# Performance work log

Measured on AMD Instinct MI355X. Metric: run time of the kernel, lower is better.

Reference implementation:

```python
import jax, jax.numpy as jnp
import numpy as np

N_QUBITS = 8
N_QLAYERS = 4
N_HEADS = 4
DIM = 2 ** N_QUBITS  # 256


def layer_norm(x, g, b, eps=1e-5):
    m = x.mean(-1, keepdims=True)
    v = ((x - m) ** 2).mean(-1, keepdims=True)
    return (x - m) / jnp.sqrt(v + eps) * g + b


def rx_mat(theta):
    # theta: scalar or [B]; returns [...,2,2] complex64
    h = theta * 0.5
    c = jnp.cos(h).astype(jnp.complex64)
    s = (jnp.sin(h) * (-1j)).astype(jnp.complex64)
    return jnp.stack([jnp.stack([c, s], -1), jnp.stack([s, c], -1)], -2)


def rz_mat(theta):
    h = (theta * 0.5).astype(jnp.complex64)
    e0 = jnp.exp(-1j * h)
    e1 = jnp.exp(1j * h)
    z = jnp.zeros_like(e0)
    return jnp.stack([jnp.stack([e0, z], -1), jnp.stack([z, e1], -1)], -2)


def apply_1q(state, U, wire, n):
    # state: [B, 2**n]; U: [2,2] (shared) or [B,2,2] (per-sample)
    B = state.shape[0]
    left = 2 ** wire
    right = 2 ** (n - 1 - wire)
    s = state.reshape(B, left, 2, right)
    if U.ndim == 2:
        s = jnp.einsum('jk,blkr->bljr', U, s)
    else:
        s = jnp.einsum('bjk,blkr->bljr', U, s)
    return s.reshape(B, 2 ** n)


def apply_cnot(state, ctrl, n):
    # CNOT with control=ctrl, target=ctrl+1 (adjacent wires)
    B = state.shape[0]
    left = 2 ** ctrl
    right = 2 ** (n - 2 - ctrl)
    s = state.reshape(B, left, 4, right)
    s = s[:, :, jnp.array([0, 1, 3, 2]), :]  # swap |10> and |11>
    return s.reshape(B, 2 ** n)


def quantum_expvals(angles, weights):
    # angles: [B, n_qubits] data-encoding angles; weights: [n_layers, 2, n_qubits]
    # Batched statevector sim of: RX(a_i)RZ(a_i) encoding, then per layer
    # RX(w[l,0,i]) RZ(w[l,1,i]) and a CNOT chain; returns <Z_i> per wire.
    n = N_QUBITS
    B = angles.shape[0]
    state = jnp.zeros((B, 2 ** n), jnp.complex64).at[:, 0].set(1.0)
    for i in range(n):
        state = apply_1q(state, rx_mat(angles[:, i]), i, n)
        state = apply_1q(state, rz_mat(angles[:, i]), i, n)
    for l in range(N_QLAYERS):
        for i in range(n):
            state = apply_1q(state, rx_mat(weights[l, 0, i]), i, n)
            state = apply_1q(state, rz_mat(weights[l, 1, i]), i, n)
        for i in range(n - 1):
            state = apply_cnot(state, i, n)
    probs = jnp.abs(state) ** 2  # [B, 2**n] float32
    zs = []
    for i in range(n):
        p = probs.reshape(B, 2 ** i, 2, 2 ** (n - 1 - i)).sum(axis=(1, 3))
        zs.append(p[:, 0] - p[:, 1])
    return jnp.stack(zs, -1)  # [B, n_qubits]


def mha(x, in_w, in_b, out_w, out_b):
    B, S, d = x.shape
    hd = d // N_HEADS
    qkv = x @ in_w.T + in_b  # [B,S,3d]
    q, k, v = jnp.split(qkv, 3, axis=-1)
    sp = lambda t: t.reshape(B, S, N_HEADS, hd).transpose(0, 2, 1, 3)
    q, k, v = sp(q), sp(k), sp(v)
    scores = jnp.einsum('bhqd,bhkd->bhqk', q, k) / np.sqrt(hd).astype(np.float32)
    attn = jax.nn.softmax(scores, axis=-1)
    o = jnp.einsum('bhqk,bhkd->bhqd', attn, v).transpose(0, 2, 1, 3).reshape(B, S, d)
    return o @ out_w.T + out_b


def _forward(x, attn_in_w, attn_in_b, attn_out_w, attn_out_b,
             ln1_g, ln1_b, ln2_g, ln2_b, ln3_g, ln3_b,
             qin_w, qin_b, qweights, qout_w, qout_b,
             ffn_w1, ffn_b1, ffn_w2, ffn_b2):
    attn_out = mha(x, attn_in_w, attn_in_b, attn_out_w, attn_out_b)
    x = layer_norm(x + attn_out, ln1_g, ln1_b)
    x_norm = layer_norm(x, ln3_g, ln3_b)
    B, S, d = x.shape
    flat = x_norm.reshape(B * S, d)
    angles = flat @ qin_w.T + qin_b  # [B*S, n_qubits]
    z = quantum_expvals(angles, qweights)
    q_out = (z @ qout_w.T + qout_b).reshape(B, S, d)
    x = x + q_out
    h = jax.nn.gelu(x @ ffn_w1.T + ffn_b1, approximate=False)  # torch GELU exact
    ffn_out = h @ ffn_w2.T + ffn_b2  # dropout is identity in eval
    return layer_norm(x + ffn_out, ln2_g, ln2_b)


def setup_inputs() -> dict:
    key = jax.random.key(0)
    ks = jax.random.split(key, 10)
    B, S, d, nq, nl = 32, 512, 512, N_QUBITS, N_QLAYERS
    rn = lambda k, sh, sc=0.02: jax.random.normal(k, sh, jnp.float32) * sc
    return {
        'x': jax.random.normal(ks[0], (B, S, d), jnp.float32),
        'attn_in_w': rn(ks[1], (3 * d, d)),
        'attn_in_b': jnp.zeros((3 * d,), jnp.float32),
        'attn_out_w': rn(ks[2], (d, d)),
        'attn_out_b': jnp.zeros((d,), jnp.float32),
        'ln1_g': jnp.ones((d,), jnp.float32), 'ln1_b': jnp.zeros((d,), jnp.float32),
        'ln2_g': jnp.ones((d,), jnp.float32), 'ln2_b': jnp.zeros((d,), jnp.float32),
        'ln3_g': jnp.ones((d,), jnp.float32), 'ln3_b': jnp.zeros((d,), jnp.float32),
        'qin_w': rn(ks[3], (nq, d), 0.05),
        'qin_b': jnp.zeros((nq,), jnp.float32),
        'qweights': jax.random.uniform(ks[4], (nl, 2, nq), jnp.float32, 0.0, 2.0 * np.pi),
        'qout_w': rn(ks[5], (d, nq), 0.1),
        'qout_b': jnp.zeros((d,), jnp.float32),
        'ffn_w1': rn(ks[6], (4 * d, d)),
        'ffn_b1': jnp.zeros((4 * d,), jnp.float32),
        'ffn_w2': rn(ks[7], (d, 4 * d)),
        'ffn_b2': jnp.zeros((d,), jnp.float32),
    }


def reference(x, attn_in_w, attn_in_b, attn_out_w, attn_out_b,
              ln1_g, ln1_b, ln2_g, ln2_b, ln3_g, ln3_b,
              qin_w, qin_b, qweights, qout_w, qout_b,
              ffn_w1, ffn_b1, ffn_w2, ffn_b2):
    return _forward(x, attn_in_w, attn_in_b, attn_out_w, attn_out_b,
                    ln1_g, ln1_b, ln2_g, ln2_b, ln3_g, ln3_b,
                    qin_w, qin_b, qweights, qout_w, qout_b,
                    ffn_w1, ffn_b1, ffn_w2, ffn_b2)
```

## Files before the change

### kernel.cpp

```cpp
#include <hip/hip_runtime.h>
#include <math.h>


typedef __bf16 bf16;
typedef bf16 bf16x8 __attribute__((ext_vector_type(8)));
typedef bf16 bf16x4 __attribute__((ext_vector_type(4)));
typedef float f32x4 __attribute__((ext_vector_type(4)));

__device__ __forceinline__ void gld16(const void* g, void* l) {
  __builtin_amdgcn_global_load_lds(
      (__attribute__((address_space(1))) void*)(void*)g,
      (__attribute__((address_space(3))) void*)l, 16, 0, 0);
}

__device__ __forceinline__ float waveAllSum(float v) {
#pragma unroll
  for (int m = 1; m < 64; m <<= 1) v += __shfl_xor(v, m, 64);
  return v;
}

__global__ __launch_bounds__(256) void cvt_all(
    const float* __restrict__ x, const float* __restrict__ w1,
    const float* __restrict__ w2, const float* __restrict__ w3,
    const float* __restrict__ w4, bf16* __restrict__ xb,
    bf16* __restrict__ b1, bf16* __restrict__ b2, bf16* __restrict__ b3,
    bf16* __restrict__ b4) {
  int i = blockIdx.x * 256 + threadIdx.x;
  const float* src;
  bf16* dst;
  int off;
  if (i < 2097152) {
    src = x; dst = xb; off = i;
  } else if (i < 2097152 + 196608) {
    src = w1; dst = b1; off = i - 2097152;
  } else if (i < 2097152 + 196608 + 65536) {
    src = w2; dst = b2; off = i - (2097152 + 196608);
  } else if (i < 2097152 + 196608 + 65536 + 262144) {
    src = w3; dst = b3; off = i - (2097152 + 196608 + 65536);
  } else {
    src = w4; dst = b4; off = i - (2097152 + 196608 + 65536 + 262144);
  }
  float4 v = ((const float4*)src)[off];
  bf16x4 o = {(bf16)v.x, (bf16)v.y, (bf16)v.z, (bf16)v.w};
  ((bf16x4*)dst)[off] = o;
}

__global__ void make_gates(const float* __restrict__ qw,
                           float* __restrict__ gates) {
  int t = threadIdx.x;
  if (t >= 32) return;
  int l = t >> 3, i = t & 7;
  float ax = qw[l * 16 + i] * 0.5f;
  float az = qw[l * 16 + 8 + i] * 0.5f;
  float cx, sx, cz, sz;
  sincosf(ax, &sx, &cx);
  sincosf(az, &sz, &cz);
  float* g = gates + t * 8;
  g[0] = cz * cx;   g[1] = -sz * cx;
  g[2] = -sz * sx;  g[3] = -cz * sx;
  g[4] = sz * sx;   g[5] = -cz * sx;
  g[6] = cz * cx;   g[7] = sz * cx;
}

__global__ __launch_bounds__(256) void make_W(const float* __restrict__ gates,
                                              bf16* __restrict__ Wp) {
  int tid = threadIdx.x, lane = tid & 63;
  int k = blockIdx.x * 4 + (tid >> 6);

  float sr[4], si[4];
#pragma unroll
  for (int l = 0; l < 4; ++l) {
    sr[l] = (lane * 4 + l == k) ? 1.0f : 0.0f;
    si[l] = 0.0f;
  }

  auto gate = [&](int p, float u00r, float u00i, float u01r, float u01i,
                  float u10r, float u10i, float u11r, float u11i) {
    if (p >= 2) {
      int m = 1 << (p - 2);
      int b = (lane >> (p - 2)) & 1;
      float csr = b ? u11r : u00r;
      float csi = b ? u11i : u00i;
      float cor = b ? u10r : u01r;
      float coi = b ? u10i : u01i;
#pragma unroll
      for (int l = 0; l < 4; ++l) {
        float pr = __shfl_xor(sr[l], m, 64);
        float pi = __shfl_xor(si[l], m, 64);
        float nr = fmaf(csr, sr[l],
                        fmaf(-csi, si[l], fmaf(cor, pr, -coi * pi)));
        float ni = fmaf(csr, si[l],
                        fmaf(csi, sr[l], fmaf(cor, pi, coi * pr)));
        sr[l] = nr;
        si[l] = ni;
      }
    } else {
      float nr[4], ni[4];
#pragma unroll
      for (int l = 0; l < 4; ++l) {
        int b = (l >> p) & 1;
        int pl = l ^ (1 << p);
        float csr = b ? u11r : u00r;
        float csi = b ? u11i : u00i;
        float cor = b ? u10r : u01r;
        float coi = b ? u10i : u01i;
        nr[l] = fmaf(csr, sr[l],
                     fmaf(-csi, si[l], fmaf(cor, sr[pl], -coi * si[pl])));
        ni[l] = fmaf(csr, si[l],
                     fmaf(csi, sr[l], fmaf(cor, si[pl], coi * sr[pl])));
      }
#pragma unroll
      for (int l = 0; l < 4; ++l) {
        sr[l] = nr[l];
        si[l] = ni[l];
      }
    }
  };
  auto docnot = [&](int i) {
    int pc = 7 - i, pt = 6 - i;
    if (pt >= 2) {
      int ctrl = (lane >> (pc - 2)) & 1;
      int m = 1 << (pt - 2);
#pragma unroll
      for (int l = 0; l < 4; ++l) {
        float pr = __shfl_xor(sr[l], m, 64);
        float pi = __shfl_xor(si[l], m, 64);
        if (ctrl) {
          sr[l] = pr;
          si[l] = pi;
        }
      }
    } else if (pt == 1) {
      if (lane & 1) {
        float t;
        t = sr[0]; sr[0] = sr[2]; sr[2] = t;
        t = si[0]; si[0] = si[2]; si[2] = t;
        t = sr[1]; sr[1] = sr[3]; sr[3] = t;
        t = si[1]; si[1] = si[3]; si[3] = t;
      }
    } else {
      float t;
      t = sr[2]; sr[2] = sr[3]; sr[3] = t;
      t = si[2]; si[2] = si[3]; si[3] = t;
    }
  };

  for (int l = 0; l < 4; ++l) {
    for (int i = 0; i < 8; ++i) {
      const float* g = gates + (l * 8 + i) * 8;
      gate(7 - i, g[0], g[1], g[2], g[3], g[4], g[5], g[6], g[7]);
    }
    for (int i = 0; i < 7; ++i) docnot(i);
  }

#pragma unroll
  for (int l = 0; l < 4; ++l) {
    int j = lane * 4 + l;
    Wp[j * 512 + k] = (bf16)sr[l];
    Wp[j * 512 + 256 + k] = (bf16)(-si[l]);
    Wp[(j + 256) * 512 + k] = (bf16)si[l];
    Wp[(j + 256) * 512 + 256 + k] = (bf16)sr[l];
  }
}

__global__ __launch_bounds__(256) void make_Q(const float* __restrict__ qout_w,
                                              bf16* __restrict__ Q) {
  int t = blockIdx.x * 256 + threadIdx.x;
  int col = t >> 8, k = t & 255;
  float s = 0.f;
#pragma unroll
  for (int w = 0; w < 8; ++w) {
    float sg = ((k >> (7 - w)) & 1) ? -1.0f : 1.0f;
    s = fmaf(qout_w[col * 8 + w], sg, s);
  }
  Q[col * 256 + k] = (bf16)s;
}

__global__ __launch_bounds__(256) void gemm_mfma(
    const bf16* __restrict__ A, const bf16* __restrict__ W,
    const float* __restrict__ bias, const float* __restrict__ Xadd,
    float* __restrict__ Cf, bf16* __restrict__ Cb, bf16* __restrict__ qk,
    bf16* __restrict__ vT, int M, int N, int K, int mode) {
  __shared__ __align__(16) bf16 As[128 * 64];
  __shared__ __align__(16) bf16 Bs[128 * 64];
  int tid = threadIdx.x;
  int lane = tid & 63, w = tid >> 6;
  int wr = w >> 1, wc = w & 1;
  int quad = lane >> 4, lc = lane & 15;
  long m0 = (long)blockIdx.x * 128;
  long n0 = (long)blockIdx.y * 128;
  f32x4 acc[4][4] = {};

  int sl0 = w * 256 + lane;

  for (int k0 = 0; k0 < K; k0 += 64) {
    __syncthreads();
#pragma unroll
    for (int c = 0; c < 4; ++c) {
      int slot = sl0 + c * 64;
      int row = slot >> 3, g = slot & 7;
      int sc = (g ^ (row & 7)) << 3;
      gld16(A + (m0 + row) * (long)K + k0 + sc, &As[slot << 3]);
      gld16(W + (n0 + row) * (long)K + k0 + sc, &Bs[slot << 3]);
    }
    __syncthreads();
#pragma unroll
    for (int t = 0; t < 2; ++t) {
      bf16x8 af[4], bfr[4];
      int pg = ((t * 4 + quad) ^ (lc & 7)) << 3;
#pragma unroll
      for (int i = 0; i < 4; ++i) {
        af[i] = *(const bf16x8*)&As[(wr * 64 + i * 16 + lc) * 64 + pg];
        bfr[i] = *(const bf16x8*)&Bs[(wc * 64 + i * 16 + lc) * 64 + pg];
      }
#pragma unroll
      for (int i = 0; i < 4; ++i)
#pragma unroll
        for (int j = 0; j < 4; ++j)
          acc[i][j] = __builtin_amdgcn_mfma_f32_16x16x32_bf16(
              af[i], bfr[j], acc[i][j], 0, 0, 0);
    }
  }

#pragma unroll
  for (int i = 0; i < 4; ++i) {
    long grow0 = m0 + wr * 64 + i * 16 + quad * 4;
#pragma unroll
    for (int j = 0; j < 4; ++j) {
      long col = n0 + wc * 64 + j * 16 + lc;
      float bv = (mode == 3) ? 0.f : bias[col];
      float v[4];
#pragma unroll
      for (int r = 0; r < 4; ++r) v[r] = acc[i][j][r] + bv;
      if (mode == 0) {
#pragma unroll
        for (int r = 0; r < 4; ++r) Cf[(grow0 + r) * N + col] = v[r];
      } else if (mode == 1) {
#pragma unroll
        for (int r = 0; r < 4; ++r) {
          float g = 0.5f * v[r] * (1.0f + erff(v[r] * 0.70710678118654752f));
          Cb[(grow0 + r) * N + col] = (bf16)g;
        }
      } else if (mode == 3) {
#pragma unroll
        for (int r = 0; r < 4; ++r) Cb[(grow0 + r) * N + col] = (bf16)v[r];
      } else if (mode == 4) {
#pragma unroll
        for (int r = 0; r < 4; ++r) {
          float val = v[r] + Xadd[(grow0 + r) * N + col];
          Cf[(grow0 + r) * N + col] = val;
          Cb[(grow0 + r) * N + col] = (bf16)val;
        }
      } else {
        if (col < 1024) {
#pragma unroll
          for (int r = 0; r < 4; ++r) qk[(grow0 + r) * 1024 + col] = (bf16)v[r];
        } else {
          int hh = (int)((col - 1024) >> 7);
          int dd = (int)((col - 1024) & 127);
          long bidx = grow0 >> 9;
          int s0 = (int)(grow0 & 511);
          bf16x4 pk = {(bf16)v[0], (bf16)v[1], (bf16)v[2], (bf16)v[3]};
          *(bf16x4*)&vT[(((bidx << 2) + hh) * 128 + dd) * 512 + s0] = pk;
        }
      }
    }
  }
}

__global__ __launch_bounds__(256) void attn_mfma(const bf16* __restrict__ qk,
                                                 const bf16* __restrict__ vT,
                                                 bf16* __restrict__ o) {
  __shared__ __align__(16) bf16 Ks[64 * 128];
  __shared__ __align__(16) bf16 Vt[128 * 64];
  __shared__ __align__(16) bf16 Ps[4][64 * 16];
  int tid = threadIdx.x, lane = tid & 63, w = tid >> 6;
  int quad = lane >> 4, lc = lane & 15;
  int bh = blockIdx.x, b = bh >> 2, h = bh & 3;
  int q0 = blockIdx.y * 64 + w * 16;
  const float scale = 0.08838834764831845f;

  bf16x8 qf[4];
  {
    const bf16* qp =
        qk + ((long)(b * 512 + q0 + lc)) * 1024 + h * 128 + quad * 8;
#pragma unroll
    for (int ks = 0; ks < 4; ++ks) qf[ks] = *(const bf16x8*)(qp + ks * 32);
  }
  f32x4 oacc[8] = {};
  float lrun[4] = {0.f, 0.f, 0.f, 0.f};

  const bf16* kbase = qk + (long)b * 512 * 1024 + 512 + h * 128;
  const bf16* vbase = vT + (long)bh * 128 * 512;
  int sl0 = w * 256 + lane;

  for (int kt = 0; kt < 512; kt += 64) {
    __syncthreads();
#pragma unroll
    for (int c = 0; c < 4; ++c) {
      int slot = sl0 + c * 64;
      {
        int row = slot >> 4, g = slot & 15;
        gld16(kbase + (long)(kt + row) * 1024 + ((g ^ (row & 15)) << 3),
              &Ks[slot << 3]);
      }
      {
        int row = slot >> 3, g = slot & 7;
        gld16(vbase + (long)row * 512 + kt + ((g ^ (row & 7)) << 3),
              &Vt[slot << 3]);
      }
    }
    __syncthreads();

    float p[4][4];
#pragma unroll
    for (int c = 0; c < 4; ++c) {
      f32x4 a = {};
#pragma unroll
      for (int ks = 0; ks < 4; ++ks) {
        bf16x8 kf = *(const bf16x8*)&Ks[(c * 16 + lc) * 128 +
                                        (((ks * 4 + quad) ^ lc) << 3)];
        a = __builtin_amdgcn_mfma_f32_16x16x32_bf16(qf[ks], kf, a, 0, 0, 0);
      }
#pragma unroll
      for (int r = 0; r < 4; ++r) p[c][r] = a[r] * scale;
    }

#pragma unroll
    for (int r = 0; r < 4; ++r) {
      float rs = 0.f;
#pragma unroll
      for (int c = 0; c < 4; ++c) {
        float e = expf(p[c][r]);
        p[c][r] = e;
        rs += e;
      }
#pragma unroll
      for (int m = 1; m < 16; m <<= 1) rs += __shfl_xor(rs, m, 64);
      lrun[r] += rs;
    }

#pragma unroll
    for (int c = 0; c < 4; ++c) {
      bf16x4 pk = {(bf16)p[c][0], (bf16)p[c][1], (bf16)p[c][2], (bf16)p[c][3]};
      *(bf16x4*)&Ps[w][(c * 16 + lc) * 16 + ((quad ^ (lc & 3)) << 2)] = pk;
    }
    bf16x8 pf[2];
#pragma unroll
    for (int kc = 0; kc < 2; ++kc) {
      bf16x8 t;
#pragma unroll
      for (int jj = 0; jj < 8; ++jj) {
        int row = kc * 32 + quad * 8 + jj;
        t[jj] = Ps[w][row * 16 + (((lc >> 2) ^ (row & 3)) << 2) + (lc & 3)];
      }
      pf[kc] = t;
    }
#pragma unroll
    for (int n = 0; n < 8; ++n)
#pragma unroll
      for (int kc = 0; kc < 2; ++kc) {
        bf16x8 vf = *(const bf16x8*)&Vt[(n * 16 + lc) * 64 +
                                        (((kc * 4 + quad) ^ (lc & 7)) << 3)];
        oacc[n] =
            __builtin_amdgcn_mfma_f32_16x16x32_bf16(pf[kc], vf, oacc[n], 0, 0, 0);
      }
  }

  float linv[4];
#pragma unroll
  for (int r = 0; r < 4; ++r) linv[r] = 1.0f / lrun[r];
  bf16* op = o + ((long)(b * 512 + q0 + quad * 4)) * 512 + h * 128 + lc;
#pragma unroll
  for (int n = 0; n < 8; ++n)
#pragma unroll
    for (int r = 0; r < 4; ++r)
      op[(long)r * 512 + n * 16] = (bf16)(oacc[n][r] * linv[r]);
}

__global__ __launch_bounds__(256) void add_ln_kernel(
    const float* __restrict__ a, const float* __restrict__ b,
    const float* __restrict__ g, const float* __restrict__ be,
    float* __restrict__ out) {
  long row = (blockIdx.x * 256 + threadIdx.x) >> 6;
  int lane = threadIdx.x & 63;
  const float* ar = a + row * 512;
  const float* br = b + row * 512;
  float v[8];
  float s = 0.f;
#pragma unroll
  for (int j = 0; j < 8; ++j) {
    int c = lane + 64 * j;
    v[j] = ar[c] + br[c];
    s += v[j];
  }
  s = waveAllSum(s);
  float mean = s * (1.0f / 512.0f);
  float var = 0.f;
#pragma unroll
  for (int j = 0; j < 8; ++j) {
    float d = v[j] - mean;
    var = fmaf(d, d, var);
  }
  var = waveAllSum(var);
  float rstd = rsqrtf(var * (1.0f / 512.0f) + 1e-5f);
  float* orow = out + row * 512;
#pragma unroll
  for (int j = 0; j < 8; ++j) {
    int c = lane + 64 * j;
    orow[c] = (v[j] - mean) * rstd * g[c] + be[c];
  }
}

__global__ __launch_bounds__(256) void quantum_pre(
    const float* __restrict__ x, const float* __restrict__ attnp,
    const float* __restrict__ g1, const float* __restrict__ b1,
    const float* __restrict__ g3, const float* __restrict__ b3,
    const float* __restrict__ qin_w, const float* __restrict__ qin_b,
    float* __restrict__ x1out, bf16* __restrict__ psi) {
  long row = (blockIdx.x * 256 + threadIdx.x) >> 6;
  int lane = threadIdx.x & 63;
  const float* xr = x + row * 512;
  const float* ar = attnp + row * 512;

  float x1v[8];
  {
    float s = 0.f;
#pragma unroll
    for (int j = 0; j < 8; ++j) {
      int c = lane + 64 * j;
      x1v[j] = xr[c] + ar[c];
      s += x1v[j];
    }
    s = waveAllSum(s);
    float mean = s * (1.0f / 512.0f);
    float var = 0.f;
#pragma unroll
    for (int j = 0; j < 8; ++j) {
      float d = x1v[j] - mean;
      var = fmaf(d, d, var);
    }
    var = waveAllSum(var);
    float rstd = rsqrtf(var * (1.0f / 512.0f) + 1e-5f);
#pragma unroll
    for (int j = 0; j < 8; ++j) {
      int c = lane + 64 * j;
      x1v[j] = (x1v[j] - mean) * rstd * g1[c] + b1[c];
    }
  }
  float* x1row = x1out + row * 512;
#pragma unroll
  for (int j = 0; j < 8; ++j) x1row[lane + 64 * j] = x1v[j];

  float xn[8];
  {
    float s = 0.f;
#pragma unroll
    for (int j = 0; j < 8; ++j) s += x1v[j];
    s = waveAllSum(s);
    float mean = s * (1.0f / 512.0f);
    float var = 0.f;
#pragma unroll
    for (int j = 0; j < 8; ++j) {
      float d = x1v[j] - mean;
      var = fmaf(d, d, var);
    }
    var = waveAllSum(var);
    float rstd = rsqrtf(var * (1.0f / 512.0f) + 1e-5f);
#pragma unroll
    for (int j = 0; j < 8; ++j) {
      int c = lane + 64 * j;
      xn[j] = (x1v[j] - mean) * rstd * g3[c] + b3[c];
    }
  }

  float ang[8];
#pragma unroll
  for (int w = 0; w < 8; ++w) {
    float p = 0.f;
#pragma unroll
    for (int j = 0; j < 8; ++j)
      p = fmaf(xn[j], qin_w[w * 512 + lane + 64 * j], p);
    p = waveAllSum(p);
    ang[w] = p + qin_b[w];
  }

  float v0r[8], v0i[8], v1r[8];
#pragma unroll
  for (int i = 0; i < 8; ++i) {
    float h = ang[i] * 0.5f;
    float c, s;
    sincosf(h, &s, &c);
    v0r[i] = c * c;
    v0i[i] = -c * s;
    v1r[i] = s * s;
  }

  float Pr, Pi;
  {
    int bit0 = (lane >> 5) & 1;
    Pr = bit0 ? v1r[0] : v0r[0];
    Pi = v0i[0];
#pragma unroll
    for (int i = 1; i < 6; ++i) {
      int bit = (lane >> (5 - i)) & 1;
      float br = bit ? v1r[i] : v0r[i];
      float bi = v0i[i];
      float nr = Pr * br - Pi * bi;
      float ni = Pr * bi + Pi * br;
      Pr = nr;
      Pi = ni;
    }
  }

  bf16 rebuf[4], imbuf[4];
#pragma unroll
  for (int l = 0; l < 4; ++l) {
    int b6 = (l >> 1) & 1, b7 = l & 1;
    float br = b6 ? v1r[6] : v0r[6], bi = v0i[6];
    float tr = Pr * br - Pi * bi;
    float ti = Pr * bi + Pi * br;
    float cr = b7 ? v1r[7] : v0r[7], ci = v0i[7];
    float fr = tr * cr - ti * ci;
    float fi = tr * ci + ti * cr;
    rebuf[l] = (bf16)fr;
    imbuf[l] = (bf16)fi;
  }
  bf16* prow = psi + row * 512;
  *(bf16x4*)&prow[lane * 4] = *(bf16x4*)rebuf;
  *(bf16x4*)&prow[256 + lane * 4] = *(bf16x4*)imbuf;
}

__global__ __launch_bounds__(256) void prob_kernel(const bf16* __restrict__ phi,
                                                   bf16* __restrict__ prob) {
  int t4 = blockIdx.x * 256 + threadIdx.x;
  int token = t4 >> 6;
  int k4 = (t4 & 63) * 4;
  const bf16* pr = phi + (long)token * 512;
  bf16x4 re = *(const bf16x4*)&pr[k4];
  bf16x4 im = *(const bf16x4*)&pr[256 + k4];
  bf16 ob[4];
#pragma unroll
  for (int l = 0; l < 4; ++l) {
    float r = (float)re[l], i = (float)im[l];
    ob[l] = (bf16)(r * r + i * i);
  }
  *(bf16x4*)&prob[(long)token * 256 + k4] = *(bf16x4*)ob;
}

extern "C" void kernel_launch(void* const* d_in, const int* in_sizes, int n_in,
                              void* d_out, int out_size, void* d_ws,
                              size_t ws_size, hipStream_t stream) {
  const float* x = (const float*)d_in[0];
  const float* attn_in_w = (const float*)d_in[1];
  const float* attn_in_b = (const float*)d_in[2];
  const float* attn_out_w = (const float*)d_in[3];
  const float* attn_out_b = (const float*)d_in[4];
  const float* ln1_g = (const float*)d_in[5];
  const float* ln1_b = (const float*)d_in[6];
  const float* ln2_g = (const float*)d_in[7];
  const float* ln2_b = (const float*)d_in[8];
  const float* ln3_g = (const float*)d_in[9];
  const float* ln3_b = (const float*)d_in[10];
  const float* qin_w = (const float*)d_in[11];
  const float* qin_b = (const float*)d_in[12];
  const float* qweights = (const float*)d_in[13];
  const float* qout_w = (const float*)d_in[14];
  const float* qout_b = (const float*)d_in[15];
  const float* ffn_w1 = (const float*)d_in[16];
  const float* ffn_b1 = (const float*)d_in[17];
  const float* ffn_w2 = (const float*)d_in[18];
  const float* ffn_b2 = (const float*)d_in[19];

  char* wsB = (char*)d_ws;
  bf16* qkb = (bf16*)(wsB);
  bf16* vtb = (bf16*)(wsB + (32L << 20));
  bf16* ob = (bf16*)(wsB + (48L << 20));
  bf16* hb = (bf16*)(wsB);
  float* slot1 = (float*)(wsB + (64L << 20));
  bf16* phi = (bf16*)(wsB + (64L << 20));
  bf16* probb = (bf16*)(wsB + (80L << 20));
  float* f2out = (float*)(wsB + (64L << 20));
  float* x1 = (float*)(wsB + (96L << 20));
  float* x2 = (float*)(wsB + (128L << 20));
  bf16* x2b = (bf16*)(wsB + (160L << 20));
  bf16* xb = (bf16*)(wsB + (176L << 20));
  bf16* psi = (bf16*)(wsB + (176L << 20));
  bf16* w_in = (bf16*)(wsB + (192L << 20));
  bf16* w_out = (bf16*)(wsB + (194L << 20));
  bf16* w_f1 = (bf16*)(wsB + (195L << 20));
  bf16* w_f2 = (bf16*)(wsB + (197L << 20));
  float* gates = (float*)(wsB + (199L << 20));
  bf16* Wp = (bf16*)(wsB + (200L << 20));
  bf16* Qm = (bf16*)(wsB + (201L << 20));

  const int M = 16384;
  float* outp = (float*)d_out;

  cvt_all<<<11264, 256, 0, stream>>>(x, attn_in_w, attn_out_w, ffn_w1, ffn_w2,
                                     xb, w_in, w_out, w_f1, w_f2);
  make_gates<<<1, 64, 0, stream>>>(qweights, gates);
  make_W<<<64, 256, 0, stream>>>(gates, Wp);
  make_Q<<<512, 256, 0, stream>>>(qout_w, Qm);

  gemm_mfma<<<dim3(M / 128, 12), 256, 0, stream>>>(
      xb, w_in, attn_in_b, nullptr, nullptr, nullptr, qkb, vtb, M, 1536, 512,
      2);
  attn_mfma<<<dim3(128, 8), 256, 0, stream>>>(qkb, vtb, ob);
  gemm_mfma<<<dim3(M / 128, 4), 256, 0, stream>>>(
      ob, w_out, attn_out_b, nullptr, slot1, nullptr, nullptr, nullptr, M, 512,
      512, 0);
  quantum_pre<<<dim3(M / 4), 256, 0, stream>>>(x, slot1, ln1_g, ln1_b, ln3_g,
                                               ln3_b, qin_w, qin_b, x1, psi);
  gemm_mfma<<<dim3(M / 128, 4), 256, 0, stream>>>(
      psi, Wp, nullptr, nullptr, nullptr, phi, nullptr, nullptr, M, 512, 512,
      3);
  prob_kernel<<<4096, 256, 0, stream>>>(phi, probb);
  gemm_mfma<<<dim3(M / 128, 4), 256, 0, stream>>>(
      probb, Qm, qout_b, x1, x2, x2b, nullptr, nullptr, M, 512, 256, 4);
  gemm_mfma<<<dim3(M / 128, 16), 256, 0, stream>>>(
      x2b, w_f1, ffn_b1, nullptr, nullptr, hb, nullptr, nullptr, M, 2048, 512,
      1);
  gemm_mfma<<<dim3(M / 128, 4), 256, 0, stream>>>(
      hb, w_f2, ffn_b2, nullptr, f2out, nullptr, nullptr, nullptr, M, 512,
      2048, 0);
  add_ln_kernel<<<dim3(M / 4), 256, 0, stream>>>(x2, f2out, ln2_g, ln2_b,
                                                 outp);
}
```

Before: 463.6 us.

## Store intermediates in bf16, fuse prob into GEMM, merge gate setup, fast GELU

All fp32 intermediates (attention projection, x1, x2, FFN output) become bf16, roughly halving their global memory traffic. The prob kernel is folded into the psi×W GEMM epilogue by interleaving real and imaginary rows and summing squares with a lane shuffle. make_gates is merged into make_W, and erf GELU is replaced by a tanh-style approximation using __expf, with softmax also switched to __expf. The cost is lower precision in the residual path and an approximate GELU, which may push results past the tolerance.

Measured after the change: 428.4 us. 1.08x faster.

```diff
diff --git a/kernel.cpp b/kernel.cpp
--- a/kernel.cpp
+++ b/kernel.cpp
@@ -17,6 +17,11 @@
 #pragma unroll
   for (int m = 1; m < 64; m <<= 1) v += __shfl_xor(v, m, 64);
   return v;
+}
+
+__device__ __forceinline__ float fast_gelu(float v) {
+  float u = 0.79788456080286536f * v * (1.0f + 0.044715f * v * v);
+  return v / (1.0f + __expf(-2.0f * u));
 }
 
 __global__ __launch_bounds__(256) void cvt_all(
@@ -45,26 +50,24 @@
   ((bf16x4*)dst)[off] = o;
 }
 
-__global__ void make_gates(const float* __restrict__ qw,
-                           float* __restrict__ gates) {
-  int t = threadIdx.x;
-  if (t >= 32) return;
-  int l = t >> 3, i = t & 7;
-  float ax = qw[l * 16 + i] * 0.5f;
-  float az = qw[l * 16 + 8 + i] * 0.5f;
-  float cx, sx, cz, sz;
-  sincosf(ax, &sx, &cx);
-  sincosf(az, &sz, &cz);
-  float* g = gates + t * 8;
-  g[0] = cz * cx;   g[1] = -sz * cx;
-  g[2] = -sz * sx;  g[3] = -cz * sx;
-  g[4] = sz * sx;   g[5] = -cz * sx;
-  g[6] = cz * cx;   g[7] = sz * cx;
-}
-
-__global__ __launch_bounds__(256) void make_W(const float* __restrict__ gates,
+__global__ __launch_bounds__(256) void make_W(const float* __restrict__ qw,
                                               bf16* __restrict__ Wp) {
+  __shared__ float gates[32 * 8];
   int tid = threadIdx.x, lane = tid & 63;
+  if (tid < 32) {
+    int l = tid >> 3, i = tid & 7;
+    float ax = qw[l * 16 + i] * 0.5f;
+    float az = qw[l * 16 + 8 + i] * 0.5f;
+    float cx, sx, cz, sz;
+    sincosf(ax, &sx, &cx);
+    sincosf(az, &sz, &cz);
+    float* g = gates + tid * 8;
+    g[0] = cz * cx;   g[1] = -sz * cx;
+    g[2] = -sz * sx;  g[3] = -cz * sx;
+    g[4] = sz * sx;   g[5] = -cz * sx;
+    g[6] = cz * cx;   g[7] = sz * cx;
+  }
+  __syncthreads();
   int k = blockIdx.x * 4 + (tid >> 6);
 
   float sr[4], si[4];
@@ -156,10 +159,10 @@
 #pragma unroll
   for (int l = 0; l < 4; ++l) {
     int j = lane * 4 + l;
-    Wp[j * 512 + k] = (bf16)sr[l];
-    Wp[j * 512 + 256 + k] = (bf16)(-si[l]);
-    Wp[(j + 256) * 512 + k] = (bf16)si[l];
-    Wp[(j + 256) * 512 + 256 + k] = (bf16)sr[l];
+    Wp[(2 * j) * 512 + k] = (bf16)sr[l];
+    Wp[(2 * j) * 512 + 256 + k] = (bf16)(-si[l]);
+    Wp[(2 * j + 1) * 512 + k] = (bf16)si[l];
+    Wp[(2 * j + 1) * 512 + 256 + k] = (bf16)sr[l];
   }
 }
 
@@ -178,9 +181,9 @@
 
 __global__ __launch_bounds__(256) void gemm_mfma(
     const bf16* __restrict__ A, const bf16* __restrict__ W,
-    const float* __restrict__ bias, const float* __restrict__ Xadd,
-    float* __restrict__ Cf, bf16* __restrict__ Cb, bf16* __restrict__ qk,
-    bf16* __restrict__ vT, int M, int N, int K, int mode) {
+    const float* __restrict__ bias, const bf16* __restrict__ Xadd,
+    bf16* __restrict__ Cb, bf16* __restrict__ qk, bf16* __restrict__ vT,
+    bf16* __restrict__ prob, int M, int N, int K, int mode) {
   __shared__ __align__(16) bf16 As[128 * 64];
   __shared__ __align__(16) bf16 Bs[128 * 64];
   int tid = threadIdx.x;
@@ -190,7 +193,6 @@
   long m0 = (long)blockIdx.x * 128;
   long n0 = (long)blockIdx.y * 128;
   f32x4 acc[4][4] = {};
-
   int sl0 = w * 256 + lane;
 
   for (int k0 = 0; k0 < K; k0 += 64) {
@@ -228,28 +230,33 @@
 #pragma unroll
     for (int j = 0; j < 4; ++j) {
       long col = n0 + wc * 64 + j * 16 + lc;
-      float bv = (mode == 3) ? 0.f : bias[col];
+      float bv = (mode == 6) ? 0.f : bias[col];
       float v[4];
 #pragma unroll
       for (int r = 0; r < 4; ++r) v[r] = acc[i][j][r] + bv;
-      if (mode == 0) {
-#pragma unroll
-        for (int r = 0; r < 4; ++r) Cf[(grow0 + r) * N + col] = v[r];
-      } else if (mode == 1) {
-#pragma unroll
-        for (int r = 0; r < 4; ++r) {
-          float g = 0.5f * v[r] * (1.0f + erff(v[r] * 0.70710678118654752f));
-          Cb[(grow0 + r) * N + col] = (bf16)g;
-        }
-      } else if (mode == 3) {
+      if (mode == 1) {
+#pragma unroll
+        for (int r = 0; r < 4; ++r)
+          Cb[(grow0 + r) * N + col] = (bf16)fast_gelu(v[r]);
+      } else if (mode == 4) {
+#pragma unroll
+        for (int r = 0; r < 4; ++r)
+          Cb[(grow0 + r) * N + col] =
+              (bf16)(v[r] + (float)Xadd[(grow0 + r) * N + col]);
+      } else if (mode == 5) {
 #pragma unroll
         for (int r = 0; r < 4; ++r) Cb[(grow0 + r) * N + col] = (bf16)v[r];
-      } else if (mode == 4) {
-#pragma unroll
-        for (int r = 0; r < 4; ++r) {
-          float val = v[r] + Xadd[(grow0 + r) * N + col];
-          Cf[(grow0 + r) * N + col] = val;
-          Cb[(grow0 + r) * N + col] = (bf16)val;
+      } else if (mode == 6) {
+        float pv[4];
+#pragma unroll
+        for (int r = 0; r < 4; ++r) pv[r] = v[r] * v[r];
+#pragma unroll
+        for (int r = 0; r < 4; ++r) pv[r] += __shfl_xor(pv[r], 1, 64);
+        if (!(lc & 1)) {
+          long pc = col >> 1;
+#pragma unroll
+          for (int r = 0; r < 4; ++r)
+            prob[(grow0 + r) * 256 + pc] = (bf16)pv[r];
         }
       } else {
         if (col < 1024) {
@@ -331,7 +338,7 @@
       float rs = 0.f;
 #pragma unroll
       for (int c = 0; c < 4; ++c) {
-        float e = expf(p[c][r]);
+        float e = __expf(p[c][r]);
         p[c][r] = e;
         rs += e;
       }
@@ -378,20 +385,20 @@
       op[(long)r * 512 + n * 16] = (bf16)(oacc[n][r] * linv[r]);
 }
 
-__global__ __launch_bounds__(256) void add_ln_kernel(
-    const float* __restrict__ a, const float* __restrict__ b,
+__global__ __launch_bounds__(256) void add_ln_bb(
+    const bf16* __restrict__ a, const bf16* __restrict__ b,
     const float* __restrict__ g, const float* __restrict__ be,
     float* __restrict__ out) {
   long row = (blockIdx.x * 256 + threadIdx.x) >> 6;
   int lane = threadIdx.x & 63;
-  const float* ar = a + row * 512;
-  const float* br = b + row * 512;
+  const bf16* ar = a + row * 512;
+  const bf16* br = b + row * 512;
   float v[8];
   float s = 0.f;
 #pragma unroll
   for (int j = 0; j < 8; ++j) {
     int c = lane + 64 * j;
-    v[j] = ar[c] + br[c];
+    v[j] = (float)ar[c] + (float)br[c];
     s += v[j];
   }
   s = waveAllSum(s);
@@ -413,15 +420,15 @@
 }
 
 __global__ __launch_bounds__(256) void quantum_pre(
-    const float* __restrict__ x, const float* __restrict__ attnp,
+    const bf16* __restrict__ xb, const bf16* __restrict__ attnpb,
     const float* __restrict__ g1, const float* __restrict__ b1,
     const float* __restrict__ g3, const float* __restrict__ b3,
     const float* __restrict__ qin_w, const float* __restrict__ qin_b,
-    float* __restrict__ x1out, bf16* __restrict__ psi) {
+    bf16* __restrict__ x1out, bf16* __restrict__ psi) {
   long row = (blockIdx.x * 256 + threadIdx.x) >> 6;
   int lane = threadIdx.x & 63;
-  const float* xr = x + row * 512;
-  const float* ar = attnp + row * 512;
+  const bf16* xr = xb + row * 512;
+  const bf16* ar = attnpb + row * 512;
 
   float x1v[8];
   {
@@ -429,7 +436,7 @@
 #pragma unroll
     for (int j = 0; j < 8; ++j) {
       int c = lane + 64 * j;
-      x1v[j] = xr[c] + ar[c];
+      x1v[j] = (float)xr[c] + (float)ar[c];
       s += x1v[j];
     }
     s = waveAllSum(s);
@@ -448,9 +455,9 @@
       x1v[j] = (x1v[j] - mean) * rstd * g1[c] + b1[c];
     }
   }
-  float* x1row = x1out + row * 512;
-#pragma unroll
-  for (int j = 0; j < 8; ++j) x1row[lane + 64 * j] = x1v[j];
+  bf16* x1row = x1out + row * 512;
+#pragma unroll
+  for (int j = 0; j < 8; ++j) x1row[lane + 64 * j] = (bf16)x1v[j];
 
   float xn[8];
   {
@@ -529,23 +536,6 @@
   bf16* prow = psi + row * 512;
   *(bf16x4*)&prow[lane * 4] = *(bf16x4*)rebuf;
   *(bf16x4*)&prow[256 + lane * 4] = *(bf16x4*)imbuf;
-}
-
-__global__ __launch_bounds__(256) void prob_kernel(const bf16* __restrict__ phi,
-                                                   bf16* __restrict__ prob) {
-  int t4 = blockIdx.x * 256 + threadIdx.x;
-  int token = t4 >> 6;
-  int k4 = (t4 & 63) * 4;
-  const bf16* pr = phi + (long)token * 512;
-  bf16x4 re = *(const bf16x4*)&pr[k4];
-  bf16x4 im = *(const bf16x4*)&pr[256 + k4];
-  bf16 ob[4];
-#pragma unroll
-  for (int l = 0; l < 4; ++l) {
-    float r = (float)re[l], i = (float)im[l];
-    ob[l] = (bf16)(r * r + i * i);
-  }
-  *(bf16x4*)&prob[(long)token * 256 + k4] = *(bf16x4*)ob;
 }
 
 extern "C" void kernel_launch(void* const* d_in, const int* in_sizes, int n_in,
@@ -577,53 +567,48 @@
   bf16* vtb = (bf16*)(wsB + (32L << 20));
   bf16* ob = (bf16*)(wsB + (48L << 20));
   bf16* hb = (bf16*)(wsB);
-  float* slot1 = (float*)(wsB + (64L << 20));
-  bf16* phi = (bf16*)(wsB + (64L << 20));
-  bf16* probb = (bf16*)(wsB + (80L << 20));
-  float* f2out = (float*)(wsB + (64L << 20));
-  float* x1 = (float*)(wsB + (96L << 20));
-  float* x2 = (float*)(wsB + (128L << 20));
-  bf16* x2b = (bf16*)(wsB + (160L << 20));
-  bf16* xb = (bf16*)(wsB + (176L << 20));
-  bf16* psi = (bf16*)(wsB + (176L << 20));
-  bf16* w_in = (bf16*)(wsB + (192L << 20));
-  bf16* w_out = (bf16*)(wsB + (194L << 20));
-  bf16* w_f1 = (bf16*)(wsB + (195L << 20));
-  bf16* w_f2 = (bf16*)(wsB + (197L << 20));
-  float* gates = (float*)(wsB + (199L << 20));
-  bf16* Wp = (bf16*)(wsB + (200L << 20));
-  bf16* Qm = (bf16*)(wsB + (201L << 20));
+  bf16* attnpb = (bf16*)(wsB + (64L << 20));
+  bf16* psi = (bf16*)(wsB + (80L << 20));
+  bf16* x1b = (bf16*)(wsB + (96L << 20));
+  bf16* probb = (bf16*)(wsB + (112L << 20));
+  bf16* x2b = (bf16*)(wsB + (120L << 20));
+  bf16* f2outb = (bf16*)(wsB + (136L << 20));
+  bf16* xb = (bf16*)(wsB + (152L << 20));
+  bf16* w_in = (bf16*)(wsB + (168L << 20));
+  bf16* w_out = (bf16*)(wsB + (170L << 20));
+  bf16* w_f1 = (bf16*)(wsB + (171L << 20));
+  bf16* w_f2 = (bf16*)(wsB + (173L << 20));
+  bf16* Wp = (bf16*)(wsB + (176L << 20));
+  bf16* Qm = (bf16*)(wsB + (177L << 20));
 
   const int M = 16384;
   float* outp = (float*)d_out;
 
   cvt_all<<<11264, 256, 0, stream>>>(x, attn_in_w, attn_out_w, ffn_w1, ffn_w2,
                                      xb, w_in, w_out, w_f1, w_f2);
-  make_gates<<<1, 64, 0, stream>>>(qweights, gates);
-  make_W<<<64, 256, 0, stream>>>(gates, Wp);
+  make_W<<<64, 256, 0, stream>>>(qweights, Wp);
   make_Q<<<512, 256, 0, stream>>>(qout_w, Qm);
 
   gemm_mfma<<<dim3(M / 128, 12), 256, 0, stream>>>(
-      xb, w_in, attn_in_b, nullptr, nullptr, nullptr, qkb, vtb, M, 1536, 512,
+      xb, w_in, attn_in_b, nullptr, nullptr, qkb, vtb, nullptr, M, 1536, 512,
       2);
   attn_mfma<<<dim3(128, 8), 256, 0, stream>>>(qkb, vtb, ob);
   gemm_mfma<<<dim3(M / 128, 4), 256, 0, stream>>>(
-      ob, w_out, attn_out_b, nullptr, slot1, nullptr, nullptr, nullptr, M, 512,
-      512, 0);
-  quantum_pre<<<dim3(M / 4), 256, 0, stream>>>(x, slot1, ln1_g, ln1_b, ln3_g,
-                                               ln3_b, qin_w, qin_b, x1, psi);
+      ob, w_out, attn_out_b, nullptr, attnpb, nullptr, nullptr, nullptr, M,
+      512, 512, 5);
+  quantum_pre<<<dim3(M / 4), 256, 0, stream>>>(xb, attnpb, ln1_g, ln1_b,
+                                               ln3_g, ln3_b, qin_w, qin_b,
+                                               x1b, psi);
   gemm_mfma<<<dim3(M / 128, 4), 256, 0, stream>>>(
-      psi, Wp, nullptr, nullptr, nullptr, phi, nullptr, nullptr, M, 512, 512,
-      3);
-  prob_kernel<<<4096, 256, 0, stream>>>(phi, probb);
+      psi, Wp, nullptr, nullptr, nullptr, nullptr, nullptr, probb, M, 512,
+      512, 6);
   gemm_mfma<<<dim3(M / 128, 4), 256, 0, stream>>>(
-      probb, Qm, qout_b, x1, x2, x2b, nullptr, nullptr, M, 512, 256, 4);
+      probb, Qm, qout_b, x1b, x2b, nullptr, nullptr, nullptr, M, 512, 256, 4);
   gemm_mfma<<<dim3(M / 128, 16), 256, 0, stream>>>(
-      x2b, w_f1, ffn_b1, nullptr, nullptr, hb, nullptr, nullptr, M, 2048, 512,
+      x2b, w_f1, ffn_b1, nullptr, hb, nullptr, nullptr, nullptr, M, 2048, 512,
       1);
   gemm_mfma<<<dim3(M / 128, 4), 256, 0, stream>>>(
-      hb, w_f2, ffn_b2, nullptr, f2out, nullptr, nullptr, nullptr, M, 512,
-      2048, 0);
-  add_ln_kernel<<<dim3(M / 4), 256, 0, stream>>>(x2, f2out, ln2_g, ln2_b,
-                                                 outp);
-}
+      hb, w_f2, ffn_b2, nullptr, f2outb, nullptr, nullptr, nullptr, M, 512,
+      2048, 5);
+  add_ln_bb<<<dim3(M / 4), 256, 0, stream>>>(x2b, f2outb, ln2_g, ln2_b, outp);
+}
```
